# Performance work log

Measured on AMD Instinct MI355X. Metric: run time of the kernel, lower is better.

Reference implementation:

```python
import jax, jax.numpy as jnp
import numpy as np

H = 768

def setup_inputs() -> dict:
    key = jax.random.key(0)
    ks = jax.random.split(key, 12)
    B, V, HID = 64, 30000, H
    s = 0.02
    return {
        "fused_features": jax.random.normal(ks[0], (B, 1, HID), jnp.float32),
        "emb":   jax.random.normal(ks[1], (V, HID), jnp.float32) * s,
        "W_ih":  jax.random.normal(ks[2], (4 * HID, HID), jnp.float32) * s,
        "W_hh":  jax.random.normal(ks[3], (4 * HID, HID), jnp.float32) * s,
        "b_ih":  jax.random.normal(ks[4], (4 * HID,), jnp.float32) * s,
        "b_hh":  jax.random.normal(ks[5], (4 * HID,), jnp.float32) * s,
        "out_W": jax.random.normal(ks[6], (V, HID), jnp.float32) * s,
        "out_b": jax.random.normal(ks[7], (V,), jnp.float32) * s,
        "c1_W":  jax.random.normal(ks[8], (512, HID), jnp.float32) * s,
        "c1_b":  jax.random.normal(ks[9], (512,), jnp.float32) * s,
        "c2_W":  jax.random.normal(ks[10], (2, 512), jnp.float32) * s,
        "c2_b":  jax.random.normal(ks[11], (2,), jnp.float32) * s,
        "max_len": 32,
    }


def _lstm_cell(x, h, c, W_ih, W_hh, b_ih, b_hh):
    # PyTorch gate order: i, f, g, o
    gates = x @ W_ih.T + b_ih + h @ W_hh.T + b_hh  # [B, 4H]
    i, f, g, o = jnp.split(gates, 4, axis=-1)
    c_new = jax.nn.sigmoid(f) * c + jax.nn.sigmoid(i) * jnp.tanh(g)
    h_new = jax.nn.sigmoid(o) * jnp.tanh(c_new)
    return h_new, c_new


def reference(fused_features, emb, W_ih, W_hh, b_ih, b_hh, out_W, out_b,
              c1_W, c1_b, c2_W, c2_b, max_len):
    B = fused_features.shape[0]
    feat = fused_features[:, 0, :]  # [B, H]

    # classifier_head: Linear(768,512) -> ReLU -> Linear(512,2)
    logits_closed = jax.nn.relu(feat @ c1_W.T + c1_b) @ c2_W.T + c2_b  # [B, 2]

    # greedy decode: start token 0, h0 = fused feature, c0 = 0
    tok0 = jnp.zeros((B,), jnp.int32)
    h0 = feat
    c0 = jnp.zeros_like(feat)

    def step(carry, _):
        tok, h, c = carry
        x = emb[tok]                                   # [B, H] embedding lookup
        h, c = _lstm_cell(x, h, c, W_ih, W_hh, b_ih, b_hh)
        logits = h @ out_W.T + out_b                   # [B, V]
        nxt = jnp.argmax(logits, axis=-1).astype(jnp.int32)
        return (nxt, h, c), nxt

    _, toks = jax.lax.scan(step, (tok0, h0, c0), None, length=max_len)
    generated = toks.T  # [B, max_len]
    return logits_closed, generated
```

## Files before the change

### kernel.cpp

```cpp
#include <hip/hip_runtime.h>
#include <math.h>
#include <float.h>
#include <limits.h>

#define BB 64
#define HID 768
#define VOCAB 30000
#define NG 3072
#define TSTEPS 32
#define PBLK 469

__global__ __launch_bounds__(256) void kc1(
    const float* __restrict__ feat, const float* __restrict__ c1W,
    const float* __restrict__ c1b, float* __restrict__ hid_ws)
{
    const int q = blockIdx.x, b = blockIdx.y;
    const int wave = threadIdx.x >> 6, lane = threadIdx.x & 63;
    float4 fr[3];
    const float4* frow = (const float4*)(feat + (size_t)b * HID);
    #pragma unroll
    for (int j = 0; j < 3; j++) fr[j] = frow[lane + 64 * j];

    #pragma unroll 2
    for (int rr = 0; rr < 32; rr++) {
        const int r = q * 128 + wave * 32 + rr;
        const float4* w = (const float4*)(c1W + (size_t)r * HID);
        float s = 0.f;
        #pragma unroll
        for (int j = 0; j < 3; j++) {
            float4 wv = w[lane + 64 * j];
            s += fr[j].x * wv.x + fr[j].y * wv.y + fr[j].z * wv.z + fr[j].w * wv.w;
        }
        #pragma unroll
        for (int o = 32; o; o >>= 1) s += __shfl_xor(s, o, 64);
        if (lane == 0) hid_ws[b * 512 + r] = fmaxf(s + c1b[r], 0.f);
    }
}

__global__ __launch_bounds__(256) void kc2(
    const float* __restrict__ hid_ws, const float* __restrict__ c2W,
    const float* __restrict__ c2b, float* __restrict__ out)
{
    const int b = blockIdx.x, tid = threadIdx.x;
    __shared__ float red[2][256];
    float s0 = 0.f, s1 = 0.f;
    for (int r = tid; r < 512; r += 256) {
        float hv = hid_ws[b * 512 + r];
        s0 += hv * c2W[r];
        s1 += hv * c2W[512 + r];
    }
    red[0][tid] = s0; red[1][tid] = s1;
    __syncthreads();
    for (int st = 128; st; st >>= 1) {
        if (tid < st) { red[0][tid] += red[0][tid + st]; red[1][tid] += red[1][tid + st]; }
        __syncthreads();
    }
    if (tid == 0) {
        out[b * 2 + 0] = red[0][0] + c2b[0];
        out[b * 2 + 1] = red[1][0] + c2b[1];
    }
}

__global__ __launch_bounds__(256) void kg1(
    int step, const int* __restrict__ tok_ws, const float* __restrict__ emb,
    const float* __restrict__ W_ih, const float* __restrict__ W_hh,
    const float* __restrict__ h_in, float* __restrict__ gpart)
{
    const int tid = threadIdx.x;
    const int nc = blockIdx.x;
    const int ks = blockIdx.y;
    __shared__ float as[64][68];
    __shared__ float wsl[64][68];
    const int ty = tid >> 4, tx = tid & 15;

    const float* abase[4];
    const float* wbase[4];
    int c4v[4], rv_[4];
    #pragma unroll
    for (int j = 0; j < 4; j++) {
        int i = tid + 256 * j;
        int r = i >> 4, c4 = i & 15;
        rv_[j] = r; c4v[j] = c4;
        if (ks < 3) {
            int tok = (step == 0) ? 0 : tok_ws[r];
            abase[j] = emb + (size_t)tok * HID + ks * 256;
        } else {
            abase[j] = h_in + (size_t)r * HID + (ks - 3) * 256;
        }
        int gcol = nc * 64 + r;
        wbase[j] = (ks < 3) ? (W_ih + (size_t)gcol * HID + ks * 256)
                            : (W_hh + (size_t)gcol * HID + (ks - 3) * 256);
    }

    float4 pa[4], pw[4];
    #pragma unroll
    for (int j = 0; j < 4; j++) {
        pa[j] = *(const float4*)(abase[j] + c4v[j] * 4);
        pw[j] = *(const float4*)(wbase[j] + c4v[j] * 4);
    }
    #pragma unroll
    for (int j = 0; j < 4; j++) {
        int r = rv_[j], cc = c4v[j] * 4;
        as[cc+0][r] = pa[j].x; as[cc+1][r] = pa[j].y; as[cc+2][r] = pa[j].z; as[cc+3][r] = pa[j].w;
        wsl[cc+0][r] = pw[j].x; wsl[cc+1][r] = pw[j].y; wsl[cc+2][r] = pw[j].z; wsl[cc+3][r] = pw[j].w;
    }

    float acc[4][4] = {};
    for (int ch = 0; ch < 4; ch++) {
        __syncthreads();
        if (ch < 3) {
            int off = (ch + 1) * 64;
            #pragma unroll
            for (int j = 0; j < 4; j++) {
                pa[j] = *(const float4*)(abase[j] + off + c4v[j] * 4);
                pw[j] = *(const float4*)(wbase[j] + off + c4v[j] * 4);
            }
        }
        #pragma unroll 16
        for (int kk = 0; kk < 64; kk++) {
            float4 av = *(const float4*)&as[kk][ty * 4];
            float4 wv = *(const float4*)&wsl[kk][tx * 4];
            acc[0][0] += av.x*wv.x; acc[0][1] += av.x*wv.y; acc[0][2] += av.x*wv.z; acc[0][3] += av.x*wv.w;
            acc[1][0] += av.y*wv.x; acc[1][1] += av.y*wv.y; acc[1][2] += av.y*wv.z; acc[1][3] += av.y*wv.w;
            acc[2][0] += av.z*wv.x; acc[2][1] += av.z*wv.y; acc[2][2] += av.z*wv.z; acc[2][3] += av.z*wv.w;
            acc[3][0] += av.w*wv.x; acc[3][1] += av.w*wv.y; acc[3][2] += av.w*wv.z; acc[3][3] += av.w*wv.w;
        }
        __syncthreads();
        if (ch < 3) {
            #pragma unroll
            for (int j = 0; j < 4; j++) {
                int r = rv_[j], cc = c4v[j] * 4;
                as[cc+0][r] = pa[j].x; as[cc+1][r] = pa[j].y; as[cc+2][r] = pa[j].z; as[cc+3][r] = pa[j].w;
                wsl[cc+0][r] = pw[j].x; wsl[cc+1][r] = pw[j].y; wsl[cc+2][r] = pw[j].z; wsl[cc+3][r] = pw[j].w;
            }
        }
    }
    #pragma unroll
    for (int i = 0; i < 4; i++) {
        float4 v = make_float4(acc[i][0], acc[i][1], acc[i][2], acc[i][3]);
        *(float4*)(gpart + ((size_t)(ks * BB) + ty * 4 + i) * NG + nc * 64 + tx * 4) = v;
    }
}

__global__ __launch_bounds__(256) void kc(
    int step, const float* __restrict__ gpart, const float* __restrict__ b_ih,
    const float* __restrict__ b_hh, float* __restrict__ cbuf, float* __restrict__ h_out)
{
    int idx = blockIdx.x * 256 + threadIdx.x;
    int b = idx / HID, j = idx % HID;
    float g4[4];
    #pragma unroll
    for (int g = 0; g < 4; g++) {
        int col = g * HID + j;
        float s = b_ih[col] + b_hh[col];
        #pragma unroll
        for (int ksd = 0; ksd < 6; ksd++)
            s += gpart[((size_t)ksd * BB + b) * NG + col];
        g4[g] = s;
    }
    float cprev = (step == 0) ? 0.f : cbuf[idx];
    float ig = 1.f / (1.f + expf(-g4[0]));
    float fg = 1.f / (1.f + expf(-g4[1]));
    float gg = tanhf(g4[2]);
    float og = 1.f / (1.f + expf(-g4[3]));
    float cn = fg * cprev + ig * gg;
    float hn = og * tanhf(cn);
    cbuf[idx] = cn;
    h_out[idx] = hn;
}

__global__ __launch_bounds__(256) void kb(
    const float* __restrict__ h, const float* __restrict__ outW,
    const float* __restrict__ outb, float* __restrict__ pval, int* __restrict__ pidx)
{
    __shared__ float hs[64][68];
    __shared__ float wsl[64][68];
    __shared__ float rv[BB][16];
    __shared__ int   ri[BB][16];
    const int tid = threadIdx.x;
    const int cb = blockIdx.x;
    const int c0 = cb * 64;
    const int ty = tid >> 4, tx = tid & 15;

    const float* abase[4];
    const float* wbase[4];
    int c4v[4], rv_[4], wok[4];
    #pragma unroll
    for (int j = 0; j < 4; j++) {
        int i = tid + 256 * j;
        int r = i >> 4, c4 = i & 15;
        rv_[j] = r; c4v[j] = c4;
        abase[j] = h + (size_t)r * HID;
        int gc = c0 + r;
        wok[j] = (gc < VOCAB);
        wbase[j] = outW + (size_t)(wok[j] ? gc : 0) * HID;
    }

    float4 pa[4], pw[4];
    const float4 z4 = make_float4(0.f, 0.f, 0.f, 0.f);
    #pragma unroll
    for (int j = 0; j < 4; j++) {
        pa[j] = *(const float4*)(abase[j] + c4v[j] * 4);
        pw[j] = wok[j] ? *(const float4*)(wbase[j] + c4v[j] * 4) : z4;
    }
    #pragma unroll
    for (int j = 0; j < 4; j++) {
        int r = rv_[j], cc = c4v[j] * 4;
        hs[cc+0][r] = pa[j].x; hs[cc+1][r] = pa[j].y; hs[cc+2][r] = pa[j].z; hs[cc+3][r] = pa[j].w;
        wsl[cc+0][r] = pw[j].x; wsl[cc+1][r] = pw[j].y; wsl[cc+2][r] = pw[j].z; wsl[cc+3][r] = pw[j].w;
    }

    float acc[4][4] = {};
    for (int ch = 0; ch < 12; ch++) {
        __syncthreads();
        if (ch < 11) {
            int off = (ch + 1) * 64;
            #pragma unroll
            for (int j = 0; j < 4; j++) {
                pa[j] = *(const float4*)(abase[j] + off + c4v[j] * 4);
                pw[j] = wok[j] ? *(const float4*)(wbase[j] + off + c4v[j] * 4) : z4;
            }
        }
        #pragma unroll 16
        for (int kk = 0; kk < 64; kk++) {
            float4 av = *(const float4*)&hs[kk][ty * 4];
            float4 wv = *(const float4*)&wsl[kk][tx * 4];
            acc[0][0] += av.x*wv.x; acc[0][1] += av.x*wv.y; acc[0][2] += av.x*wv.z; acc[0][3] += av.x*wv.w;
            acc[1][0] += av.y*wv.x; acc[1][1] += av.y*wv.y; acc[1][2] += av.y*wv.z; acc[1][3] += av.y*wv.w;
            acc[2][0] += av.z*wv.x; acc[2][1] += av.z*wv.y; acc[2][2] += av.z*wv.z; acc[2][3] += av.z*wv.w;
            acc[3][0] += av.w*wv.x; acc[3][1] += av.w*wv.y; acc[3][2] += av.w*wv.z; acc[3][3] += av.w*wv.w;
        }
        __syncthreads();
        if (ch < 11) {
            #pragma unroll
            for (int j = 0; j < 4; j++) {
                int r = rv_[j], cc = c4v[j] * 4;
                hs[cc+0][r] = pa[j].x; hs[cc+1][r] = pa[j].y; hs[cc+2][r] = pa[j].z; hs[cc+3][r] = pa[j].w;
                wsl[cc+0][r] = pw[j].x; wsl[cc+1][r] = pw[j].y; wsl[cc+2][r] = pw[j].z; wsl[cc+3][r] = pw[j].w;
            }
        }
    }

    #pragma unroll
    for (int i = 0; i < 4; i++) {
        float bv = -FLT_MAX; int bi = INT_MAX;
        #pragma unroll
        for (int j = 0; j < 4; j++) {
            int c = c0 + tx * 4 + j;
            if (c < VOCAB) {
                float v = acc[i][j] + outb[c];
                if (v > bv || (v == bv && c < bi)) { bv = v; bi = c; }
            }
        }
        rv[ty * 4 + i][tx] = bv; ri[ty * 4 + i][tx] = bi;
    }
    __syncthreads();
    if (tid < BB) {
        float bv = -FLT_MAX; int bi = INT_MAX;
        #pragma unroll
        for (int x = 0; x < 16; x++) {
            float v = rv[tid][x]; int ix = ri[tid][x];
            if (v > bv || (v == bv && ix < bi)) { bv = v; bi = ix; }
        }
        pval[tid * PBLK + cb] = bv;
        pidx[tid * PBLK + cb] = bi;
    }
}

__global__ __launch_bounds__(256) void kfin(
    int step, const float* __restrict__ pval, const int* __restrict__ pidx,
    int* __restrict__ tok_ws, float* __restrict__ gen)
{
    const int b = blockIdx.x, tid = threadIdx.x;
    __shared__ float sv[256];
    __shared__ int   si[256];
    float bv = -FLT_MAX; int bi = INT_MAX;
    for (int p = tid; p < PBLK; p += 256) {
        float v = pval[b * PBLK + p]; int ix = pidx[b * PBLK + p];
        if (v > bv || (v == bv && ix < bi)) { bv = v; bi = ix; }
    }
    sv[tid] = bv; si[tid] = bi;
    __syncthreads();
    for (int st = 128; st; st >>= 1) {
        if (tid < st) {
            float v = sv[tid + st]; int ix = si[tid + st];
            if (v > sv[tid] || (v == sv[tid] && ix < si[tid])) { sv[tid] = v; si[tid] = ix; }
        }
        __syncthreads();
    }
    if (tid == 0) {
        tok_ws[b] = si[0];
        gen[b * TSTEPS + step] = (float)si[0];
    }
}

extern "C" void kernel_launch(void* const* d_in, const int* in_sizes, int n_in,
                              void* d_out, int out_size, void* d_ws, size_t ws_size,
                              hipStream_t stream)
{
    const float* feat = (const float*)d_in[0];
    const float* emb  = (const float*)d_in[1];
    const float* W_ih = (const float*)d_in[2];
    const float* W_hh = (const float*)d_in[3];
    const float* b_ih = (const float*)d_in[4];
    const float* b_hh = (const float*)d_in[5];
    const float* outW = (const float*)d_in[6];
    const float* outb = (const float*)d_in[7];
    const float* c1W  = (const float*)d_in[8];
    const float* c1b  = (const float*)d_in[9];
    const float* c2W  = (const float*)d_in[10];
    const float* c2b  = (const float*)d_in[11];
    (void)in_sizes; (void)n_in; (void)out_size; (void)ws_size;

    float* out = (float*)d_out;
    float* gen = out + BB * 2;

    float* ws     = (float*)d_ws;
    float* hbuf   = ws;
    float* cbuf   = hbuf + 2 * BB * HID;
    float* gpart  = cbuf + BB * HID;
    float* pval   = gpart + 6 * (size_t)BB * NG;
    int*   pidx   = (int*)(pval + BB * PBLK);
    int*   tok    = pidx + BB * PBLK;
    float* hid_ws = (float*)(tok + BB);

    kc1<<<dim3(4, BB), 256, 0, stream>>>(feat, c1W, c1b, hid_ws);
    kc2<<<BB, 256, 0, stream>>>(hid_ws, c2W, c2b, out);

    for (int t = 0; t < TSTEPS; t++) {
        const float* h_in = (t == 0) ? feat : (hbuf + ((t - 1) & 1) * BB * HID);
        float* h_out = hbuf + (t & 1) * BB * HID;
        kg1<<<dim3(48, 6), 256, 0, stream>>>(t, tok, emb, W_ih, W_hh, h_in, gpart);
        kc<<<dim3(192), 256, 0, stream>>>(t, gpart, b_ih, b_hh, cbuf, h_out);
        kb<<<dim3(PBLK), 256, 0, stream>>>(h_out, outW, outb, pval, pidx);
        kfin<<<BB, 256, 0, stream>>>(t, pval, pidx, tok, gen);
    }
}
```

Measured before the change: 3.423 ms.

## Restructure LSTM decode into wave-per-column GEMV kernels with transposed activations

Replaces the LDS-tiled GEMM kernels with wave-per-output kernels that keep activations transposed ([H][64]), so each lane handles one batch row and weight loads are wave-uniform scalar/broadcast reads. The gate kernel fuses the split-K partial sums, the bias and the LSTM cell, which removes the gpart buffer and the separate reduction kernel. The final argmax kernel also gathers the next embedding into the transposed layout. The risk is that wave-uniform weight reads with no data reuse across waves may be limited by scalar load throughput instead of using the memory bandwidth efficiently.

```diff
diff --git a/kernel.cpp b/kernel.cpp
--- a/kernel.cpp
+++ b/kernel.cpp
@@ -6,9 +6,10 @@
 #define BB 64
 #define HID 768
 #define VOCAB 30000
-#define NG 3072
 #define TSTEPS 32
-#define PBLK 469
+#define CPW 8
+#define NWAVE (VOCAB / CPW)
+#define NBLK ((NWAVE + 3) / 4)
 
 __global__ __launch_bounds__(256) void kc1(
     const float* __restrict__ feat, const float* __restrict__ c1W,
@@ -61,222 +62,115 @@
     }
 }
 
-__global__ __launch_bounds__(256) void kg1(
-    int step, const int* __restrict__ tok_ws, const float* __restrict__ emb,
+__global__ __launch_bounds__(256) void kprep(
+    const float* __restrict__ feat, const float* __restrict__ emb,
+    float* __restrict__ hA, float* __restrict__ xT)
+{
+    int idx = blockIdx.x * 256 + threadIdx.x;
+    int k = idx >> 6, b = idx & 63;
+    hA[idx] = feat[b * HID + k];
+    xT[idx] = emb[k];
+}
+
+__global__ __launch_bounds__(256) void kgate(
+    int step, const float* __restrict__ xT, const float* __restrict__ hT_in,
     const float* __restrict__ W_ih, const float* __restrict__ W_hh,
-    const float* __restrict__ h_in, float* __restrict__ gpart)
-{
-    const int tid = threadIdx.x;
-    const int nc = blockIdx.x;
-    const int ks = blockIdx.y;
-    __shared__ float as[64][68];
-    __shared__ float wsl[64][68];
-    const int ty = tid >> 4, tx = tid & 15;
-
-    const float* abase[4];
-    const float* wbase[4];
-    int c4v[4], rv_[4];
-    #pragma unroll
-    for (int j = 0; j < 4; j++) {
-        int i = tid + 256 * j;
-        int r = i >> 4, c4 = i & 15;
-        rv_[j] = r; c4v[j] = c4;
-        if (ks < 3) {
-            int tok = (step == 0) ? 0 : tok_ws[r];
-            abase[j] = emb + (size_t)tok * HID + ks * 256;
-        } else {
-            abase[j] = h_in + (size_t)r * HID + (ks - 3) * 256;
-        }
-        int gcol = nc * 64 + r;
-        wbase[j] = (ks < 3) ? (W_ih + (size_t)gcol * HID + ks * 256)
-                            : (W_hh + (size_t)gcol * HID + (ks - 3) * 256);
-    }
-
-    float4 pa[4], pw[4];
-    #pragma unroll
-    for (int j = 0; j < 4; j++) {
-        pa[j] = *(const float4*)(abase[j] + c4v[j] * 4);
-        pw[j] = *(const float4*)(wbase[j] + c4v[j] * 4);
-    }
-    #pragma unroll
-    for (int j = 0; j < 4; j++) {
-        int r = rv_[j], cc = c4v[j] * 4;
-        as[cc+0][r] = pa[j].x; as[cc+1][r] = pa[j].y; as[cc+2][r] = pa[j].z; as[cc+3][r] = pa[j].w;
-        wsl[cc+0][r] = pw[j].x; wsl[cc+1][r] = pw[j].y; wsl[cc+2][r] = pw[j].z; wsl[cc+3][r] = pw[j].w;
-    }
-
-    float acc[4][4] = {};
-    for (int ch = 0; ch < 4; ch++) {
-        __syncthreads();
-        if (ch < 3) {
-            int off = (ch + 1) * 64;
-            #pragma unroll
-            for (int j = 0; j < 4; j++) {
-                pa[j] = *(const float4*)(abase[j] + off + c4v[j] * 4);
-                pw[j] = *(const float4*)(wbase[j] + off + c4v[j] * 4);
-            }
-        }
-        #pragma unroll 16
-        for (int kk = 0; kk < 64; kk++) {
-            float4 av = *(const float4*)&as[kk][ty * 4];
-            float4 wv = *(const float4*)&wsl[kk][tx * 4];
-            acc[0][0] += av.x*wv.x; acc[0][1] += av.x*wv.y; acc[0][2] += av.x*wv.z; acc[0][3] += av.x*wv.w;
-            acc[1][0] += av.y*wv.x; acc[1][1] += av.y*wv.y; acc[1][2] += av.y*wv.z; acc[1][3] += av.y*wv.w;
-            acc[2][0] += av.z*wv.x; acc[2][1] += av.z*wv.y; acc[2][2] += av.z*wv.z; acc[2][3] += av.z*wv.w;
-            acc[3][0] += av.w*wv.x; acc[3][1] += av.w*wv.y; acc[3][2] += av.w*wv.z; acc[3][3] += av.w*wv.w;
-        }
-        __syncthreads();
-        if (ch < 3) {
-            #pragma unroll
-            for (int j = 0; j < 4; j++) {
-                int r = rv_[j], cc = c4v[j] * 4;
-                as[cc+0][r] = pa[j].x; as[cc+1][r] = pa[j].y; as[cc+2][r] = pa[j].z; as[cc+3][r] = pa[j].w;
-                wsl[cc+0][r] = pw[j].x; wsl[cc+1][r] = pw[j].y; wsl[cc+2][r] = pw[j].z; wsl[cc+3][r] = pw[j].w;
-            }
-        }
-    }
-    #pragma unroll
-    for (int i = 0; i < 4; i++) {
-        float4 v = make_float4(acc[i][0], acc[i][1], acc[i][2], acc[i][3]);
-        *(float4*)(gpart + ((size_t)(ks * BB) + ty * 4 + i) * NG + nc * 64 + tx * 4) = v;
-    }
-}
-
-__global__ __launch_bounds__(256) void kc(
-    int step, const float* __restrict__ gpart, const float* __restrict__ b_ih,
-    const float* __restrict__ b_hh, float* __restrict__ cbuf, float* __restrict__ h_out)
-{
-    int idx = blockIdx.x * 256 + threadIdx.x;
-    int b = idx / HID, j = idx % HID;
-    float g4[4];
-    #pragma unroll
-    for (int g = 0; g < 4; g++) {
-        int col = g * HID + j;
-        float s = b_ih[col] + b_hh[col];
-        #pragma unroll
-        for (int ksd = 0; ksd < 6; ksd++)
-            s += gpart[((size_t)ksd * BB + b) * NG + col];
-        g4[g] = s;
-    }
-    float cprev = (step == 0) ? 0.f : cbuf[idx];
-    float ig = 1.f / (1.f + expf(-g4[0]));
-    float fg = 1.f / (1.f + expf(-g4[1]));
-    float gg = tanhf(g4[2]);
-    float og = 1.f / (1.f + expf(-g4[3]));
+    const float* __restrict__ b_ih, const float* __restrict__ b_hh,
+    float* __restrict__ cT, float* __restrict__ hT_out)
+{
+    const int lane = threadIdx.x & 63;
+    const int j = __builtin_amdgcn_readfirstlane((blockIdx.x << 2) | (threadIdx.x >> 6));
+
+    float acc[4];
+    #pragma unroll
+    for (int g = 0; g < 4; g++) acc[g] = b_ih[g * HID + j] + b_hh[g * HID + j];
+
+    for (int k0 = 0; k0 < HID; k0 += 16) {
+        float xv[16];
+        #pragma unroll
+        for (int kk = 0; kk < 16; kk++) xv[kk] = xT[(k0 + kk) * 64 + lane];
+        #pragma unroll
+        for (int g = 0; g < 4; g++) {
+            const float* w = W_ih + (size_t)(g * HID + j) * HID + k0;
+            #pragma unroll
+            for (int kk = 0; kk < 16; kk++) acc[g] = fmaf(xv[kk], w[kk], acc[g]);
+        }
+    }
+    for (int k0 = 0; k0 < HID; k0 += 16) {
+        float hv[16];
+        #pragma unroll
+        for (int kk = 0; kk < 16; kk++) hv[kk] = hT_in[(k0 + kk) * 64 + lane];
+        #pragma unroll
+        for (int g = 0; g < 4; g++) {
+            const float* w = W_hh + (size_t)(g * HID + j) * HID + k0;
+            #pragma unroll
+            for (int kk = 0; kk < 16; kk++) acc[g] = fmaf(hv[kk], w[kk], acc[g]);
+        }
+    }
+
+    float cprev = (step == 0) ? 0.f : cT[j * 64 + lane];
+    float ig = 1.f / (1.f + expf(-acc[0]));
+    float fg = 1.f / (1.f + expf(-acc[1]));
+    float gg = tanhf(acc[2]);
+    float og = 1.f / (1.f + expf(-acc[3]));
     float cn = fg * cprev + ig * gg;
     float hn = og * tanhf(cn);
-    cbuf[idx] = cn;
-    h_out[idx] = hn;
-}
-
-__global__ __launch_bounds__(256) void kb(
-    const float* __restrict__ h, const float* __restrict__ outW,
+    cT[j * 64 + lane] = cn;
+    hT_out[j * 64 + lane] = hn;
+}
+
+__global__ __launch_bounds__(256) void klog(
+    const float* __restrict__ hT, const float* __restrict__ outW,
     const float* __restrict__ outb, float* __restrict__ pval, int* __restrict__ pidx)
 {
-    __shared__ float hs[64][68];
-    __shared__ float wsl[64][68];
-    __shared__ float rv[BB][16];
-    __shared__ int   ri[BB][16];
-    const int tid = threadIdx.x;
-    const int cb = blockIdx.x;
-    const int c0 = cb * 64;
-    const int ty = tid >> 4, tx = tid & 15;
-
-    const float* abase[4];
-    const float* wbase[4];
-    int c4v[4], rv_[4], wok[4];
-    #pragma unroll
-    for (int j = 0; j < 4; j++) {
-        int i = tid + 256 * j;
-        int r = i >> 4, c4 = i & 15;
-        rv_[j] = r; c4v[j] = c4;
-        abase[j] = h + (size_t)r * HID;
-        int gc = c0 + r;
-        wok[j] = (gc < VOCAB);
-        wbase[j] = outW + (size_t)(wok[j] ? gc : 0) * HID;
-    }
-
-    float4 pa[4], pw[4];
-    const float4 z4 = make_float4(0.f, 0.f, 0.f, 0.f);
-    #pragma unroll
-    for (int j = 0; j < 4; j++) {
-        pa[j] = *(const float4*)(abase[j] + c4v[j] * 4);
-        pw[j] = wok[j] ? *(const float4*)(wbase[j] + c4v[j] * 4) : z4;
-    }
-    #pragma unroll
-    for (int j = 0; j < 4; j++) {
-        int r = rv_[j], cc = c4v[j] * 4;
-        hs[cc+0][r] = pa[j].x; hs[cc+1][r] = pa[j].y; hs[cc+2][r] = pa[j].z; hs[cc+3][r] = pa[j].w;
-        wsl[cc+0][r] = pw[j].x; wsl[cc+1][r] = pw[j].y; wsl[cc+2][r] = pw[j].z; wsl[cc+3][r] = pw[j].w;
-    }
-
-    float acc[4][4] = {};
-    for (int ch = 0; ch < 12; ch++) {
-        __syncthreads();
-        if (ch < 11) {
-            int off = (ch + 1) * 64;
-            #pragma unroll
-            for (int j = 0; j < 4; j++) {
-                pa[j] = *(const float4*)(abase[j] + off + c4v[j] * 4);
-                pw[j] = wok[j] ? *(const float4*)(wbase[j] + off + c4v[j] * 4) : z4;
-            }
-        }
-        #pragma unroll 16
-        for (int kk = 0; kk < 64; kk++) {
-            float4 av = *(const float4*)&hs[kk][ty * 4];
-            float4 wv = *(const float4*)&wsl[kk][tx * 4];
-            acc[0][0] += av.x*wv.x; acc[0][1] += av.x*wv.y; acc[0][2] += av.x*wv.z; acc[0][3] += av.x*wv.w;
-            acc[1][0] += av.y*wv.x; acc[1][1] += av.y*wv.y; acc[1][2] += av.y*wv.z; acc[1][3] += av.y*wv.w;
-            acc[2][0] += av.z*wv.x; acc[2][1] += av.z*wv.y; acc[2][2] += av.z*wv.z; acc[2][3] += av.z*wv.w;
-            acc[3][0] += av.w*wv.x; acc[3][1] += av.w*wv.y; acc[3][2] += av.w*wv.z; acc[3][3] += av.w*wv.w;
-        }
-        __syncthreads();
-        if (ch < 11) {
-            #pragma unroll
-            for (int j = 0; j < 4; j++) {
-                int r = rv_[j], cc = c4v[j] * 4;
-                hs[cc+0][r] = pa[j].x; hs[cc+1][r] = pa[j].y; hs[cc+2][r] = pa[j].z; hs[cc+3][r] = pa[j].w;
-                wsl[cc+0][r] = pw[j].x; wsl[cc+1][r] = pw[j].y; wsl[cc+2][r] = pw[j].z; wsl[cc+3][r] = pw[j].w;
-            }
-        }
-    }
-
-    #pragma unroll
-    for (int i = 0; i < 4; i++) {
-        float bv = -FLT_MAX; int bi = INT_MAX;
-        #pragma unroll
-        for (int j = 0; j < 4; j++) {
-            int c = c0 + tx * 4 + j;
-            if (c < VOCAB) {
-                float v = acc[i][j] + outb[c];
-                if (v > bv || (v == bv && c < bi)) { bv = v; bi = c; }
-            }
-        }
-        rv[ty * 4 + i][tx] = bv; ri[ty * 4 + i][tx] = bi;
-    }
-    __syncthreads();
-    if (tid < BB) {
-        float bv = -FLT_MAX; int bi = INT_MAX;
-        #pragma unroll
-        for (int x = 0; x < 16; x++) {
-            float v = rv[tid][x]; int ix = ri[tid][x];
-            if (v > bv || (v == bv && ix < bi)) { bv = v; bi = ix; }
-        }
-        pval[tid * PBLK + cb] = bv;
-        pidx[tid * PBLK + cb] = bi;
-    }
+    const int lane = threadIdx.x & 63;
+    const int wid = __builtin_amdgcn_readfirstlane((blockIdx.x << 2) | (threadIdx.x >> 6));
+    if (wid >= NWAVE) return;
+    const int n0 = wid * CPW;
+
+    float acc[CPW] = {};
+    float hv[16], hn[16];
+    #pragma unroll
+    for (int kk = 0; kk < 16; kk++) hv[kk] = hT[kk * 64 + lane];
+
+    for (int k0 = 0; k0 < HID; k0 += 16) {
+        if (k0 + 16 < HID) {
+            #pragma unroll
+            for (int kk = 0; kk < 16; kk++) hn[kk] = hT[(k0 + 16 + kk) * 64 + lane];
+        }
+        #pragma unroll
+        for (int c = 0; c < CPW; c++) {
+            const float* w = outW + (size_t)(n0 + c) * HID + k0;
+            #pragma unroll
+            for (int kk = 0; kk < 16; kk++) acc[c] = fmaf(hv[kk], w[kk], acc[c]);
+        }
+        if (k0 + 16 < HID) {
+            #pragma unroll
+            for (int kk = 0; kk < 16; kk++) hv[kk] = hn[kk];
+        }
+    }
+
+    float bv = -FLT_MAX; int bi = INT_MAX;
+    #pragma unroll
+    for (int c = 0; c < CPW; c++) {
+        float v = acc[c] + outb[n0 + c];
+        if (v > bv) { bv = v; bi = n0 + c; }
+    }
+    pval[lane * NWAVE + wid] = bv;
+    pidx[lane * NWAVE + wid] = bi;
 }
 
 __global__ __launch_bounds__(256) void kfin(
     int step, const float* __restrict__ pval, const int* __restrict__ pidx,
-    int* __restrict__ tok_ws, float* __restrict__ gen)
+    const float* __restrict__ emb, float* __restrict__ xT, float* __restrict__ gen)
 {
     const int b = blockIdx.x, tid = threadIdx.x;
     __shared__ float sv[256];
     __shared__ int   si[256];
+    __shared__ int   stok;
     float bv = -FLT_MAX; int bi = INT_MAX;
-    for (int p = tid; p < PBLK; p += 256) {
-        float v = pval[b * PBLK + p]; int ix = pidx[b * PBLK + p];
+    for (int p = tid; p < NWAVE; p += 256) {
+        float v = pval[b * NWAVE + p]; int ix = pidx[b * NWAVE + p];
         if (v > bv || (v == bv && ix < bi)) { bv = v; bi = ix; }
     }
     sv[tid] = bv; si[tid] = bi;
@@ -289,9 +183,13 @@
         __syncthreads();
     }
     if (tid == 0) {
-        tok_ws[b] = si[0];
+        stok = si[0];
         gen[b * TSTEPS + step] = (float)si[0];
     }
+    __syncthreads();
+    const int tok = stok;
+    for (int k = tid; k < HID; k += 256)
+        xT[k * 64 + b] = emb[(size_t)tok * HID + k];
 }
 
 extern "C" void kernel_launch(void* const* d_in, const int* in_sizes, int n_in,
@@ -316,23 +214,23 @@
     float* gen = out + BB * 2;
 
     float* ws     = (float*)d_ws;
-    float* hbuf   = ws;
-    float* cbuf   = hbuf + 2 * BB * HID;
-    float* gpart  = cbuf + BB * HID;
-    float* pval   = gpart + 6 * (size_t)BB * NG;
-    int*   pidx   = (int*)(pval + BB * PBLK);
-    int*   tok    = pidx + BB * PBLK;
-    float* hid_ws = (float*)(tok + BB);
+    float* hA     = ws;
+    float* hB     = hA + HID * 64;
+    float* cT     = hB + HID * 64;
+    float* xT     = cT + HID * 64;
+    float* pval   = xT + HID * 64;
+    int*   pidx   = (int*)(pval + BB * NWAVE);
+    float* hid_ws = (float*)(pidx + BB * NWAVE);
 
     kc1<<<dim3(4, BB), 256, 0, stream>>>(feat, c1W, c1b, hid_ws);
     kc2<<<BB, 256, 0, stream>>>(hid_ws, c2W, c2b, out);
+    kprep<<<dim3(HID * 64 / 256), 256, 0, stream>>>(feat, emb, hA, xT);
 
     for (int t = 0; t < TSTEPS; t++) {
-        const float* h_in = (t == 0) ? feat : (hbuf + ((t - 1) & 1) * BB * HID);
-        float* h_out = hbuf + (t & 1) * BB * HID;
-        kg1<<<dim3(48, 6), 256, 0, stream>>>(t, tok, emb, W_ih, W_hh, h_in, gpart);
-        kc<<<dim3(192), 256, 0, stream>>>(t, gpart, b_ih, b_hh, cbuf, h_out);
-        kb<<<dim3(PBLK), 256, 0, stream>>>(h_out, outW, outb, pval, pidx);
-        kfin<<<BB, 256, 0, stream>>>(t, pval, pidx, tok, gen);
-    }
-}
+        const float* h_in = (t & 1) ? hB : hA;
+        float*       h_out = (t & 1) ? hA : hB;
+        kgate<<<dim3(192), 256, 0, stream>>>(t, xT, h_in, W_ih, W_hh, b_ih, b_hh, cT, h_out);
+        klog<<<dim3(NBLK), 256, 0, stream>>>(h_out, outW, outb, pval, pidx);
+        kfin<<<BB, 256, 0, stream>>>(t, pval, pidx, emb, xT, gen);
+    }
+}
```

Result: slower. 6.070 ms (+77.3%).
